# Performance work log

Hardware: AMD Instinct MI355X
Metric: run time of the kernel (lower is better)

The kernel has to match this reference:

```python
import jax, jax.numpy as jnp
import numpy as np

B, N, C, H = 8, 2048, 768, 12
HD = C // H
SCALE = HD ** -0.5


def setup_inputs() -> dict:
    key = jax.random.key(0)
    ks = jax.random.split(key, 10)
    x = jax.random.normal(ks[0], (B, N, C), dtype=jnp.float32)
    size = jax.random.uniform(ks[1], (B, N, 1), dtype=jnp.float32, minval=0.1, maxval=8.0)
    def lin(k):
        return jax.random.normal(k, (C, C), dtype=jnp.float32) * 0.02
    return {
        "x": x,
        "size": size,
        "q_w": lin(ks[2]), "q_b": jnp.zeros((C,), jnp.float32),
        "k_w": lin(ks[3]), "k_b": jnp.zeros((C,), jnp.float32),
        "v_w": lin(ks[4]), "v_b": jnp.zeros((C,), jnp.float32),
        "o_w": lin(ks[5]), "o_b": jnp.zeros((C,), jnp.float32),
    }


def reference(x, size, q_w, q_b, k_w, k_b, v_w, v_b, o_w, o_b):
    # q/k/v projections: [B,N,C] -> [B,H,N,hd]
    def proj(w, b):
        y = jnp.einsum('bnc,dc->bnd', x, w) + b
        return y.reshape(B, N, H, HD).transpose(0, 2, 1, 3)
    q = proj(q_w, q_b)
    k = proj(k_w, k_b)
    v = proj(v_w, v_b)
    # scores with additive log-size bias on keys: [B,H,N,N]
    attn = jnp.einsum('bhqd,bhkd->bhqk', q, k) * SCALE
    attn = attn + jnp.log(size)[:, None, None, :, 0]
    attn = jax.nn.softmax(attn, axis=-1)
    out = jnp.einsum('bhqk,bhkd->bhqd', attn, v)
    out = out.transpose(0, 2, 1, 3).reshape(B, N, C)
    out = jnp.einsum('bnc,dc->bnd', out, o_w) + o_b
    return out, k.mean(axis=1)
```

## Files before the change

kernel.cpp:

```cpp
#include <hip/hip_runtime.h>
#include <math.h>

constexpr int BB = 8, NN = 2048, CC = 768, HH = 12, DD = 64;
constexpr float SCALE2 = 0.18033688011112042f;
constexpr long long BNC = (long long)BB * NN * CC;
constexpr long long WN  = 589824LL;
constexpr long long XN  = BNC;

using bf16x8  = __attribute__((ext_vector_type(8))) __bf16;
using floatx4 = __attribute__((ext_vector_type(4))) float;
using f16x4   = __attribute__((ext_vector_type(4))) _Float16;
using f16x8   = __attribute__((ext_vector_type(8))) _Float16;

static __device__ __forceinline__ unsigned short f2bf(float x) {
  unsigned u = __builtin_bit_cast(unsigned, x);
  u += 0x7fffu + ((u >> 16) & 1u);
  return (unsigned short)(u >> 16);
}
static __device__ __forceinline__ float bf2f(unsigned short s) {
  unsigned u = ((unsigned)s) << 16;
  return __builtin_bit_cast(float, u);
}

static __device__ __forceinline__ void async_copy16(const unsigned short* g, unsigned short* l) {
  __builtin_amdgcn_global_load_lds(
      (const __attribute__((address_space(1))) unsigned int*)g,
      (__attribute__((address_space(3))) unsigned int*)l, 16, 0, 0);
}

__global__ void convert_kernel(const float* __restrict__ x,
    const float* __restrict__ qw, const float* __restrict__ kw,
    const float* __restrict__ vw, const float* __restrict__ ow,
    const float* __restrict__ qb, const float* __restrict__ kb,
    const float* __restrict__ vb,
    unsigned short* __restrict__ xb, unsigned short* __restrict__ wcat,
    unsigned short* __restrict__ owb, float* __restrict__ bcat) {
  const long long gid = (long long)blockIdx.x * 256 + threadIdx.x;
  const long long off = gid * 4;
  if (off < XN + 4 * WN) {
    const float* s; unsigned short* d;
    if (off < XN)              { s = x  + off;                 d = xb   + off; }
    else if (off < XN + WN)    { s = qw + (off - XN);          d = wcat + (off - XN); }
    else if (off < XN + 2*WN)  { s = kw + (off - XN - WN);     d = wcat + (off - XN); }
    else if (off < XN + 3*WN)  { s = vw + (off - XN - 2*WN);   d = wcat + (off - XN); }
    else                       { s = ow + (off - XN - 3*WN);   d = owb  + (off - XN - 3*WN); }
    floatx4 v = *(const floatx4*)s;
    union { unsigned short us[4]; unsigned long long u; } pk;
    pk.us[0] = f2bf(v.x); pk.us[1] = f2bf(v.y); pk.us[2] = f2bf(v.z); pk.us[3] = f2bf(v.w);
    *(unsigned long long*)d = pk.u;
  } else {
    long long r = gid - (XN + 4 * WN) / 4;
    if (r < 576) {
      long long o2 = r * 4;
      const float* s = (o2 < 768) ? qb + o2 : (o2 < 1536) ? kb + (o2 - 768) : vb + (o2 - 1536);
      *(floatx4*)(bcat + o2) = *(const floatx4*)s;
    }
  }
}

template<int OUT_MODE>
__global__ __launch_bounds__(256, 3)
void gemm_m97(const unsigned short* __restrict__ A,
              const unsigned short* __restrict__ Bw,
              const float* __restrict__ bias,
              unsigned short* __restrict__ Qo,
              unsigned short* __restrict__ Ko,
              unsigned short* __restrict__ Vo,
              float* __restrict__ Fo) {
  __shared__ __align__(16) unsigned short As[128 * 64];
  __shared__ __align__(16) unsigned short Bs[128 * 64];
  const int t    = threadIdx.x;
  const int lane = t & 63;
  const int wv   = t >> 6;
  const int q    = lane >> 4;
  const int ml   = lane & 15;
  const int wm   = wv >> 1, wn = wv & 1;
  const int m0   = blockIdx.x * 128;
  const int n0   = blockIdx.y * 128;
  const int scol = ((lane & 7) ^ (lane >> 3)) * 8;

  const unsigned short* Ag = A  + (size_t)(m0 + wv * 32 + (lane >> 3)) * CC + scol;
  const unsigned short* Bg = Bw + (size_t)(n0 + wv * 32 + (lane >> 3)) * CC + scol;
  unsigned short* Al = As + (wv * 32) * 64;
  unsigned short* Bl = Bs + (wv * 32) * 64;

  floatx4 acc[4][4] = {};

  for (int k0 = 0; k0 < CC; k0 += 64) {
    #pragma unroll
    for (int i = 0; i < 4; ++i) {
      async_copy16(Ag + (size_t)i * 8 * CC + k0, Al + i * 8 * 64);
      async_copy16(Bg + (size_t)i * 8 * CC + k0, Bl + i * 8 * 64);
    }
    __syncthreads();
    #pragma unroll
    for (int kk = 0; kk < 2; ++kk) {
      bf16x8 af[4], bg[4];
      #pragma unroll
      for (int mt = 0; mt < 4; ++mt) {
        const int ch = ((kk * 4 + q) ^ (ml & 7)) * 8;
        af[mt] = *(const bf16x8*)&As[(wm * 64 + mt * 16 + ml) * 64 + ch];
      }
      #pragma unroll
      for (int nt = 0; nt < 4; ++nt) {
        const int ch = ((kk * 4 + q) ^ (ml & 7)) * 8;
        bg[nt] = *(const bf16x8*)&Bs[(wn * 64 + nt * 16 + ml) * 64 + ch];
      }
      #pragma unroll
      for (int mt = 0; mt < 4; ++mt)
        #pragma unroll
        for (int nt = 0; nt < 4; ++nt)
          acc[mt][nt] = __builtin_amdgcn_mfma_f32_16x16x32_bf16(af[mt], bg[nt], acc[mt][nt], 0, 0, 0);
    }
    __syncthreads();
  }

  #pragma unroll
  for (int nt = 0; nt < 4; ++nt) {
    const int col = n0 + wn * 64 + nt * 16 + ml;
    const float bv = bias[col];
    #pragma unroll
    for (int mt = 0; mt < 4; ++mt) {
      const int mbase = m0 + wm * 64 + mt * 16 + q * 4;
      if (OUT_MODE == 1) {
        #pragma unroll
        for (int r = 0; r < 4; ++r)
          Fo[(size_t)(mbase + r) * CC + col] = acc[mt][nt][r] + bv;
      } else {
        const int region = blockIdx.y / 6;
        const int lc = col - region * CC;
        const int h = lc >> 6, hd = lc & 63;
        const int bidx = mbase >> 11;
        if (region == 2) {
          const int nloc  = mbase & (NN - 1);
          const int pbase = (nloc & ~127) + (((nloc >> 2) & 3) << 5) + (((nloc >> 4) & 7) << 2);
          union { _Float16 h4[4]; unsigned long long u; } pk;
          #pragma unroll
          for (int r = 0; r < 4; ++r) pk.h4[r] = (_Float16)(acc[mt][nt][r] + bv);
          *(unsigned long long*)&Vo[((size_t)(bidx * HH + h) * DD + hd) * NN + pbase] = pk.u;
        } else {
          const int n = mbase & (NN - 1);
          unsigned short* o = (region == 0) ? Qo : Ko;
          #pragma unroll
          for (int r = 0; r < 4; ++r)
            o[((size_t)(bidx * HH + h) * NN + n + r) * DD + hd] = f2bf(acc[mt][nt][r] + bv);
        }
      }
    }
  }
}

__global__ __launch_bounds__(256, 2)
void attn_kernel(const unsigned short* __restrict__ Qp,
                 const unsigned short* __restrict__ Kp,
                 const unsigned short* __restrict__ Vt,
                 const float* __restrict__ sz,
                 unsigned short* __restrict__ attn_out) {
  __shared__ __align__(16) unsigned short Ks[2][128 * 64];
  __shared__ __align__(16) unsigned short Vs[2][64 * 128];
  __shared__ __align__(16) float biasS[2][128];

  const int t    = threadIdx.x;
  const int lane = t & 63;
  const int wv   = t >> 6;
  const int q    = lane >> 4;
  const int ml   = lane & 15;
  const int wg   = (blockIdx.x & 7) * 192 + (blockIdx.x >> 3);
  const int bh   = wg >> 4;
  const int qt   = wg & 15;
  const int b    = bh / HH, h = bh % HH;
  const int qbase = qt * 128 + wv * 32;

  bf16x8 qf[2][2];
  #pragma unroll
  for (int mq = 0; mq < 2; ++mq)
    #pragma unroll
    for (int kt = 0; kt < 2; ++kt)
      qf[mq][kt] = *(const bf16x8*)(Qp + ((size_t)bh * NN + qbase + mq * 16 + ml) * DD + kt * 32 + q * 8);

  floatx4 O[2][4] = {};
  floatx4 Osum[2] = {};
  f16x4 vone = {(_Float16)1.f, (_Float16)1.f, (_Float16)1.f, (_Float16)1.f};

  const int kswz = ((lane & 7) ^ (lane >> 3)) * 8;
  const int vswz = ((lane & 15) ^ (lane >> 4)) * 8;
  const unsigned short* Kg = Kp + ((size_t)bh * NN + wv * 32 + (lane >> 3)) * DD + kswz;
  const unsigned short* Vg = Vt + ((size_t)bh * DD + wv * 16 + (lane >> 4)) * NN;

  #pragma unroll
  for (int i = 0; i < 4; ++i) {
    async_copy16(Kg + (size_t)(i * 8) * DD, &Ks[0][(wv * 32) * 64] + i * 8 * 64);
    async_copy16(Vg + (size_t)(i * 4) * NN + (vswz ^ ((i & 1) << 5)), &Vs[0][(wv * 16) * 128] + i * 4 * 128);
  }
  float szreg = 0.f;
  if (t < 128) {
    biasS[0][t] = log2f(sz[(size_t)b * NN + t]);
    szreg = sz[(size_t)b * NN + 128 + t];
  }
  __syncthreads();

  auto do_tile = [&](int jt, int cur, int nxt) {
    const int j0 = jt * 128;

    if (jt < 15) {
      const int jn = j0 + 128;
      #pragma unroll
      for (int i = 0; i < 4; ++i) {
        async_copy16(Kg + (size_t)(jn + i * 8) * DD, &Ks[nxt][(wv * 32) * 64] + i * 8 * 64);
        async_copy16(Vg + (size_t)(i * 4) * NN + jn + (vswz ^ ((i & 1) << 5)),
                     &Vs[nxt][(wv * 16) * 128] + i * 4 * 128);
      }
      if (t < 128) {
        biasS[nxt][t] = log2f(szreg);
        int j2 = jn + 128; if (j2 + 128 > NN) j2 = NN - 128;
        szreg = sz[(size_t)b * NN + j2 + t];
      }
    }

    floatx4 bfr[8];
    #pragma unroll
    for (int nt = 0; nt < 8; ++nt)
      bfr[nt] = *(const floatx4*)&biasS[cur][nt * 16 + q * 4];

    floatx4 S[2][8];
    __builtin_amdgcn_s_setprio(1);
    #pragma unroll
    for (int nt = 0; nt < 8; ++nt) {
      const int ch0 = (q ^ (ml & 7)) * 8;
      const int ch1 = ((4 + q) ^ (ml & 7)) * 8;
      bf16x8 kf0 = *(const bf16x8*)&Ks[cur][(nt * 16 + ml) * 64 + ch0];
      bf16x8 kf1 = *(const bf16x8*)&Ks[cur][(nt * 16 + ml) * 64 + ch1];
      #pragma unroll
      for (int mq = 0; mq < 2; ++mq) {
        floatx4 a = {0.f, 0.f, 0.f, 0.f};
        a = __builtin_amdgcn_mfma_f32_16x16x32_bf16(kf0, qf[mq][0], a, 0, 0, 0);
        a = __builtin_amdgcn_mfma_f32_16x16x32_bf16(kf1, qf[mq][1], a, 0, 0, 0);
        S[mq][nt] = a;
      }
    }
    __builtin_amdgcn_s_setprio(0);

    f16x4 pf[2][8];
    #pragma unroll
    for (int mq = 0; mq < 2; ++mq)
      #pragma unroll
      for (int nt = 0; nt < 8; ++nt)
        #pragma unroll
        for (int r = 0; r < 4; ++r)
          pf[mq][nt][r] = (_Float16)__builtin_amdgcn_exp2f(fmaf(S[mq][nt][r], SCALE2, bfr[nt][r]));

    __builtin_amdgcn_s_setprio(1);
    #pragma unroll
    for (int dt = 0; dt < 4; ++dt) {
      #pragma unroll
      for (int tt = 0; tt < 4; ++tt) {
        const int ch = ((q * 4 + tt) ^ (ml & 7)) * 8;
        f16x8 vv = *(const f16x8*)&Vs[cur][(dt * 16 + ml) * 128 + ch];
        f16x4 va = __builtin_shufflevector(vv, vv, 0, 1, 2, 3);
        f16x4 vb = __builtin_shufflevector(vv, vv, 4, 5, 6, 7);
        #pragma unroll
        for (int mq = 0; mq < 2; ++mq) {
          O[mq][dt] = __builtin_amdgcn_mfma_f32_16x16x16f16(va, pf[mq][2 * tt],     O[mq][dt], 0, 0, 0);
          O[mq][dt] = __builtin_amdgcn_mfma_f32_16x16x16f16(vb, pf[mq][2 * tt + 1], O[mq][dt], 0, 0, 0);
        }
      }
    }
    #pragma unroll
    for (int mq = 0; mq < 2; ++mq)
      #pragma unroll
      for (int nt = 0; nt < 8; ++nt)
        Osum[mq] = __builtin_amdgcn_mfma_f32_16x16x16f16(vone, pf[mq][nt], Osum[mq], 0, 0, 0);
    __builtin_amdgcn_s_setprio(0);

    __syncthreads();
  };

  for (int jt = 0; jt < 16; jt += 2) {
    do_tile(jt, 0, 1);
    do_tile(jt + 1, 1, 0);
  }

  #pragma unroll
  for (int mq = 0; mq < 2; ++mq) {
    const float linv = 1.0f / Osum[mq][0];
    const int query = qbase + mq * 16 + ml;
    #pragma unroll
    for (int dt = 0; dt < 4; ++dt) {
      union { unsigned short us[4]; unsigned long long u; } pk;
      #pragma unroll
      for (int r = 0; r < 4; ++r) pk.us[r] = f2bf(O[mq][dt][r] * linv);
      *(unsigned long long*)&attn_out[((size_t)b * NN + query) * CC + h * DD + dt * 16 + q * 4] = pk.u;
    }
  }
}

__global__ void kmean_kernel(const unsigned short* __restrict__ Kp, float* __restrict__ o) {
  int idx = blockIdx.x * 256 + threadIdx.x;
  int hd4 = (idx & 15) << 2;
  int n   = (idx >> 4) & (NN - 1);
  int b   = idx >> 15;
  float s0 = 0.f, s1 = 0.f, s2 = 0.f, s3 = 0.f;
  #pragma unroll
  for (int h = 0; h < HH; ++h) {
    ushort4 u = *(const ushort4*)&Kp[(((size_t)b * HH + h) * NN + n) * DD + hd4];
    s0 += bf2f(u.x); s1 += bf2f(u.y); s2 += bf2f(u.z); s3 += bf2f(u.w);
  }
  float4 r;
  r.x = s0 * (1.0f / 12.0f); r.y = s1 * (1.0f / 12.0f);
  r.z = s2 * (1.0f / 12.0f); r.w = s3 * (1.0f / 12.0f);
  *(float4*)&o[(size_t)idx * 4] = r;
}

extern "C" void kernel_launch(void* const* d_in, const int* in_sizes, int n_in,
                              void* d_out, int out_size, void* d_ws, size_t ws_size,
                              hipStream_t stream) {
  const float* x   = (const float*)d_in[0];
  const float* sz  = (const float*)d_in[1];
  const float* q_w = (const float*)d_in[2];
  const float* q_b = (const float*)d_in[3];
  const float* k_w = (const float*)d_in[4];
  const float* k_b = (const float*)d_in[5];
  const float* v_w = (const float*)d_in[6];
  const float* v_b = (const float*)d_in[7];
  const float* o_w = (const float*)d_in[8];
  const float* o_b = (const float*)d_in[9];

  float* out0  = (float*)d_out;
  float* outKm = out0 + (size_t)BNC;

  unsigned short* xb   = (unsigned short*)d_ws;
  unsigned short* wcat = xb + XN;
  unsigned short* owb  = wcat + 3 * WN;
  float*          bcat = (float*)(owb + WN);
  unsigned short* Qw   = (unsigned short*)(bcat + 2304);
  unsigned short* Kw   = Qw + BNC;
  unsigned short* Vtw  = Kw + BNC;
  unsigned short* Aw   = xb;

  dim3 tb(256, 1, 1);
  convert_kernel<<<dim3(14595), tb, 0, stream>>>(x, q_w, k_w, v_w, o_w, q_b, k_b, v_b,
                                                 xb, wcat, owb, bcat);
  gemm_m97<0><<<dim3(128, 18), tb, 0, stream>>>(xb, wcat, bcat, Qw, Kw, Vtw, nullptr);
  attn_kernel<<<dim3(BB * HH * 16), tb, 0, stream>>>(Qw, Kw, Vtw, sz, Aw);
  gemm_m97<1><<<dim3(128, 6), tb, 0, stream>>>(Aw, owb, o_b, nullptr, nullptr, nullptr, out0);
  kmean_kernel<<<dim3(1024), tb, 0, stream>>>(Kw, outKm);
}
```

Before: 368.9 us.

## Widen GEMM tiles to 512 threads and single-buffer V in attention

```diff
diff --git a/kernel.cpp b/kernel.cpp
--- a/kernel.cpp
+++ b/kernel.cpp
@@ -59,7 +59,7 @@
 }
 
 template<int OUT_MODE>
-__global__ __launch_bounds__(256, 3)
+__global__ __launch_bounds__(512, 4)
 void gemm_m97(const unsigned short* __restrict__ A,
               const unsigned short* __restrict__ Bw,
               const float* __restrict__ bias,
@@ -68,30 +68,31 @@
               unsigned short* __restrict__ Vo,
               float* __restrict__ Fo) {
   __shared__ __align__(16) unsigned short As[128 * 64];
-  __shared__ __align__(16) unsigned short Bs[128 * 64];
+  __shared__ __align__(16) unsigned short Bs[256 * 64];
   const int t    = threadIdx.x;
   const int lane = t & 63;
   const int wv   = t >> 6;
   const int q    = lane >> 4;
   const int ml   = lane & 15;
-  const int wm   = wv >> 1, wn = wv & 1;
+  const int wm   = wv >> 2, wn = wv & 3;
   const int m0   = blockIdx.x * 128;
-  const int n0   = blockIdx.y * 128;
+  const int n0   = blockIdx.y * 256;
   const int scol = ((lane & 7) ^ (lane >> 3)) * 8;
 
-  const unsigned short* Ag = A  + (size_t)(m0 + wv * 32 + (lane >> 3)) * CC + scol;
+  const unsigned short* Ag = A  + (size_t)(m0 + wv * 16 + (lane >> 3)) * CC + scol;
   const unsigned short* Bg = Bw + (size_t)(n0 + wv * 32 + (lane >> 3)) * CC + scol;
-  unsigned short* Al = As + (wv * 32) * 64;
+  unsigned short* Al = As + (wv * 16) * 64;
   unsigned short* Bl = Bs + (wv * 32) * 64;
 
   floatx4 acc[4][4] = {};
 
   for (int k0 = 0; k0 < CC; k0 += 64) {
     #pragma unroll
-    for (int i = 0; i < 4; ++i) {
+    for (int i = 0; i < 2; ++i)
       async_copy16(Ag + (size_t)i * 8 * CC + k0, Al + i * 8 * 64);
+    #pragma unroll
+    for (int i = 0; i < 4; ++i)
       async_copy16(Bg + (size_t)i * 8 * CC + k0, Bl + i * 8 * 64);
-    }
     __syncthreads();
     #pragma unroll
     for (int kk = 0; kk < 2; ++kk) {
@@ -127,7 +128,7 @@
         for (int r = 0; r < 4; ++r)
           Fo[(size_t)(mbase + r) * CC + col] = acc[mt][nt][r] + bv;
       } else {
-        const int region = blockIdx.y / 6;
+        const int region = blockIdx.y / 3;
         const int lc = col - region * CC;
         const int h = lc >> 6, hd = lc & 63;
         const int bidx = mbase >> 11;
@@ -150,14 +151,14 @@
   }
 }
 
-__global__ __launch_bounds__(256, 2)
+__global__ __launch_bounds__(256, 3)
 void attn_kernel(const unsigned short* __restrict__ Qp,
                  const unsigned short* __restrict__ Kp,
                  const unsigned short* __restrict__ Vt,
                  const float* __restrict__ sz,
                  unsigned short* __restrict__ attn_out) {
   __shared__ __align__(16) unsigned short Ks[2][128 * 64];
-  __shared__ __align__(16) unsigned short Vs[2][64 * 128];
+  __shared__ __align__(16) unsigned short Vs[64 * 128];
   __shared__ __align__(16) float biasS[2][128];
 
   const int t    = threadIdx.x;
@@ -180,17 +181,21 @@
 
   floatx4 O[2][4] = {};
   floatx4 Osum[2] = {};
-  f16x4 vone = {(_Float16)1.f, (_Float16)1.f, (_Float16)1.f, (_Float16)1.f};
+  f16x8 vone8 = {(_Float16)1.f, (_Float16)1.f, (_Float16)1.f, (_Float16)1.f,
+                 (_Float16)1.f, (_Float16)1.f, (_Float16)1.f, (_Float16)1.f};
 
   const int kswz = ((lane & 7) ^ (lane >> 3)) * 8;
   const int vswz = ((lane & 15) ^ (lane >> 4)) * 8;
   const unsigned short* Kg = Kp + ((size_t)bh * NN + wv * 32 + (lane >> 3)) * DD + kswz;
   const unsigned short* Vg = Vt + ((size_t)bh * DD + wv * 16 + (lane >> 4)) * NN;
+  unsigned short* Kl0 = &Ks[0][(wv * 32) * 64];
+  unsigned short* Kl1 = &Ks[1][(wv * 32) * 64];
+  unsigned short* Vl  = Vs + (wv * 16) * 128;
 
   #pragma unroll
   for (int i = 0; i < 4; ++i) {
-    async_copy16(Kg + (size_t)(i * 8) * DD, &Ks[0][(wv * 32) * 64] + i * 8 * 64);
-    async_copy16(Vg + (size_t)(i * 4) * NN + (vswz ^ ((i & 1) << 5)), &Vs[0][(wv * 16) * 128] + i * 4 * 128);
+    async_copy16(Kg + (size_t)(i * 8) * DD, Kl0 + i * 8 * 64);
+    async_copy16(Vg + (size_t)(i * 4) * NN + (vswz ^ ((i & 1) << 5)), Vl + i * 4 * 128);
   }
   float szreg = 0.f;
   if (t < 128) {
@@ -199,19 +204,18 @@
   }
   __syncthreads();
 
-  auto do_tile = [&](int jt, int cur, int nxt) {
-    const int j0 = jt * 128;
+  for (int jt = 0; jt < 16; ++jt) {
+    const int cur = jt & 1;
+    const int j0  = jt * 128;
+    const int jn  = j0 + 128;
+    unsigned short* Kln = cur ? Kl0 : Kl1;
 
     if (jt < 15) {
-      const int jn = j0 + 128;
-      #pragma unroll
-      for (int i = 0; i < 4; ++i) {
-        async_copy16(Kg + (size_t)(jn + i * 8) * DD, &Ks[nxt][(wv * 32) * 64] + i * 8 * 64);
-        async_copy16(Vg + (size_t)(i * 4) * NN + jn + (vswz ^ ((i & 1) << 5)),
-                     &Vs[nxt][(wv * 16) * 128] + i * 4 * 128);
-      }
+      #pragma unroll
+      for (int i = 0; i < 4; ++i)
+        async_copy16(Kg + (size_t)(jn + i * 8) * DD, Kln + i * 8 * 64);
       if (t < 128) {
-        biasS[nxt][t] = log2f(szreg);
+        biasS[cur ^ 1][t] = log2f(szreg);
         int j2 = jn + 128; if (j2 + 128 > NN) j2 = NN - 128;
         szreg = sz[(size_t)b * NN + j2 + t];
       }
@@ -240,14 +244,19 @@
     }
     __builtin_amdgcn_s_setprio(0);
 
-    f16x4 pf[2][8];
+    f16x8 pfw[2][4];
     #pragma unroll
     for (int mq = 0; mq < 2; ++mq)
       #pragma unroll
-      for (int nt = 0; nt < 8; ++nt)
+      for (int tt = 0; tt < 4; ++tt)
         #pragma unroll
-        for (int r = 0; r < 4; ++r)
-          pf[mq][nt][r] = (_Float16)__builtin_amdgcn_exp2f(fmaf(S[mq][nt][r], SCALE2, bfr[nt][r]));
+        for (int bb = 0; bb < 2; ++bb)
+          #pragma unroll
+          for (int r = 0; r < 4; ++r)
+            pfw[mq][tt][bb * 4 + r] =
+                (_Float16)__builtin_amdgcn_exp2f(fmaf(S[mq][2 * tt + bb][r], SCALE2, bfr[2 * tt + bb][r]));
+
+    __syncthreads();
 
     __builtin_amdgcn_s_setprio(1);
     #pragma unroll
@@ -255,29 +264,29 @@
       #pragma unroll
       for (int tt = 0; tt < 4; ++tt) {
         const int ch = ((q * 4 + tt) ^ (ml & 7)) * 8;
-        f16x8 vv = *(const f16x8*)&Vs[cur][(dt * 16 + ml) * 128 + ch];
-        f16x4 va = __builtin_shufflevector(vv, vv, 0, 1, 2, 3);
-        f16x4 vb = __builtin_shufflevector(vv, vv, 4, 5, 6, 7);
+        f16x8 vv = *(const f16x8*)&Vs[(dt * 16 + ml) * 128 + ch];
         #pragma unroll
-        for (int mq = 0; mq < 2; ++mq) {
-          O[mq][dt] = __builtin_amdgcn_mfma_f32_16x16x16f16(va, pf[mq][2 * tt],     O[mq][dt], 0, 0, 0);
-          O[mq][dt] = __builtin_amdgcn_mfma_f32_16x16x16f16(vb, pf[mq][2 * tt + 1], O[mq][dt], 0, 0, 0);
-        }
-      }
-    }
+        for (int mq = 0; mq < 2; ++mq)
+          O[mq][dt] = __builtin_amdgcn_mfma_f32_16x16x32_f16(vv, pfw[mq][tt], O[mq][dt], 0, 0, 0);
+      }
+    }
+    __builtin_amdgcn_s_setprio(0);
+
+    __syncthreads();
+
+    if (jt < 15) {
+      #pragma unroll
+      for (int i = 0; i < 4; ++i)
+        async_copy16(Vg + (size_t)(i * 4) * NN + jn + (vswz ^ ((i & 1) << 5)), Vl + i * 4 * 128);
+    }
+
+    __builtin_amdgcn_s_setprio(1);
     #pragma unroll
     for (int mq = 0; mq < 2; ++mq)
       #pragma unroll
-      for (int nt = 0; nt < 8; ++nt)
-        Osum[mq] = __builtin_amdgcn_mfma_f32_16x16x16f16(vone, pf[mq][nt], Osum[mq], 0, 0, 0);
+      for (int tt = 0; tt < 4; ++tt)
+        Osum[mq] = __builtin_amdgcn_mfma_f32_16x16x32_f16(vone8, pfw[mq][tt], Osum[mq], 0, 0, 0);
     __builtin_amdgcn_s_setprio(0);
-
-    __syncthreads();
-  };
-
-  for (int jt = 0; jt < 16; jt += 2) {
-    do_tile(jt, 0, 1);
-    do_tile(jt + 1, 1, 0);
   }
 
   #pragma unroll
@@ -338,10 +347,11 @@
   unsigned short* Aw   = xb;
 
   dim3 tb(256, 1, 1);
+  dim3 tg(512, 1, 1);
   convert_kernel<<<dim3(14595), tb, 0, stream>>>(x, q_w, k_w, v_w, o_w, q_b, k_b, v_b,
                                                  xb, wcat, owb, bcat);
-  gemm_m97<0><<<dim3(128, 18), tb, 0, stream>>>(xb, wcat, bcat, Qw, Kw, Vtw, nullptr);
+  gemm_m97<0><<<dim3(128, 9), tg, 0, stream>>>(xb, wcat, bcat, Qw, Kw, Vtw, nullptr);
   attn_kernel<<<dim3(BB * HH * 16), tb, 0, stream>>>(Qw, Kw, Vtw, sz, Aw);
-  gemm_m97<1><<<dim3(128, 6), tb, 0, stream>>>(Aw, owb, o_b, nullptr, nullptr, nullptr, out0);
+  gemm_m97<1><<<dim3(128, 3), tg, 0, stream>>>(Aw, owb, o_b, nullptr, nullptr, nullptr, out0);
   kmean_kernel<<<dim3(1024), tb, 0, stream>>>(Kw, outKm);
 }
```

New measurement: 390.0 us. 5.7% more time.
